# Optimization experiments

Hardware: AMD Instinct MI355X
Metric: run time of the kernel (lower is better)

The kernel has to match this reference:

```python
import jax, jax.numpy as jnp
import numpy as np

N_NODES = 100000
N_EDGES = 1600000


def gcn_conv(x, src, dst, W, b, n_nodes):
    # PyG GCNConv: h = x @ W; symmetric normalization with self-loops; scatter-add; + bias
    deg = jax.ops.segment_sum(jnp.ones_like(src, dtype=x.dtype), dst, num_segments=n_nodes)
    dinv = jax.lax.rsqrt(jnp.where(deg > 0, deg, 1.0))
    norm = dinv[src] * dinv[dst]              # [E+N]
    h = x @ W                                  # [N, out]
    msg = h[src] * norm[:, None]               # gather + scale (irregular access)
    out = jax.ops.segment_sum(msg, dst, num_segments=n_nodes)  # scatter-add aggregate
    return out + b


def setup_inputs() -> dict:
    key = jax.random.key(0)
    k1, k2, k3, k4 = jax.random.split(key, 4)
    x = jax.random.normal(k1, (N_NODES, 128), dtype=jnp.float32)
    edge_index = jax.random.randint(k2, (2, N_EDGES), 0, N_NODES, dtype=jnp.int64)
    W1 = jax.random.normal(k3, (128, 48), dtype=jnp.float32) * (1.0 / np.sqrt(128))
    b1 = jnp.zeros((48,), dtype=jnp.float32)
    W2 = jax.random.normal(k4, (48, 16), dtype=jnp.float32) * (1.0 / np.sqrt(48))
    b2 = jnp.zeros((16,), dtype=jnp.float32)
    return {"x": x, "edge_index": edge_index, "W1": W1, "b1": b1, "W2": W2, "b2": b2}


def reference(x, edge_index, W1, b1, W2, b2):
    n = x.shape[0]
    loops = jnp.arange(n, dtype=edge_index.dtype)
    src = jnp.concatenate([edge_index[0], loops])  # add self-loops
    dst = jnp.concatenate([edge_index[1], loops])
    h = gcn_conv(x, src, dst, W1, b1, n)
    h = jax.nn.relu(h)
    h = gcn_conv(h, src, dst, W2, b2, n)
    h = jax.nn.relu(h)
    return jax.nn.softmax(h, axis=1)
```

## Files before the change

kernel.cpp:

```cpp
#include <hip/hip_runtime.h>
#include <hip/hip_bf16.h>
#include <hip/hip_fp16.h>


#define TILE 4096

typedef _Float16 half8 __attribute__((ext_vector_type(8)));
typedef float floatx4 __attribute__((ext_vector_type(4)));

__global__ __launch_bounds__(256) void k_bhist(const int* __restrict__ dst, int E,
                                               int* __restrict__ Hw, int nbuck) {
    __shared__ int h[512];
    int t = threadIdx.x;
    for (int i = t; i < nbuck; i += 256) h[i] = 0;
    __syncthreads();
    int base = blockIdx.x * TILE;
#pragma unroll
    for (int r = 0; r < TILE / 1024; ++r) {
        int e = base + (r * 256 + t) * 4;
        if (e + 3 < E) {
            int4 d4 = *(const int4*)(dst + e);
            atomicAdd(&h[d4.x >> 8], 1);
            atomicAdd(&h[d4.y >> 8], 1);
            atomicAdd(&h[d4.z >> 8], 1);
            atomicAdd(&h[d4.w >> 8], 1);
        } else {
            for (int k = 0; k < 4; ++k)
                if (e + k < E) atomicAdd(&h[dst[e + k] >> 8], 1);
        }
    }
    __syncthreads();
    for (int i = t; i < nbuck; i += 256) Hw[blockIdx.x * nbuck + i] = h[i];
}

__global__ __launch_bounds__(256) void k_bsum(const int* __restrict__ Hw, int nTiles,
                                              int nbuck, int* __restrict__ btot) {
    int wid = (blockIdx.x * 256 + threadIdx.x) >> 6;
    int lane = threadIdx.x & 63;
    if (wid >= nbuck) return;
    int sum = 0;
    for (int tt = lane; tt < nTiles; tt += 64) sum += Hw[tt * nbuck + wid];
#pragma unroll
    for (int off = 32; off; off >>= 1) sum += __shfl_down(sum, off);
    if (lane == 0) btot[wid] = sum;
}

__global__ __launch_bounds__(256) void k_boff(int* __restrict__ Hw, int nTiles,
                                              int nbuck, const int* __restrict__ btot,
                                              int* __restrict__ bstart) {
    int wid = (blockIdx.x * 256 + threadIdx.x) >> 6;
    int lane = threadIdx.x & 63;
    if (wid >= nbuck) return;
    int ps = 0;
    for (int j = lane; j < wid; j += 64) ps += btot[j];
#pragma unroll
    for (int off = 32; off; off >>= 1) ps += __shfl_down(ps, off);
    int prefix = __shfl(ps, 0);
    if (lane == 0) {
        bstart[wid] = prefix;
        if (wid == nbuck - 1) bstart[nbuck] = prefix + btot[wid];
    }
    int running = prefix;
    for (int chunk = 0; chunk < nTiles; chunk += 64) {
        int tt = chunk + lane;
        int v = (tt < nTiles) ? Hw[tt * nbuck + wid] : 0;
        int incl = v;
#pragma unroll
        for (int off = 1; off < 64; off <<= 1) {
            int u = __shfl_up(incl, off);
            if (lane >= off) incl += u;
        }
        if (tt < nTiles) Hw[tt * nbuck + wid] = running + (incl - v);
        running += __shfl(incl, 63);
    }
}

__global__ __launch_bounds__(256) void k_bscatter(const int* __restrict__ ei, int E,
                                                  const int* __restrict__ Hw, int nbuck,
                                                  int* __restrict__ ebuf) {
    __shared__ int cur[512];
    int t = threadIdx.x;
    for (int i = t; i < nbuck; i += 256) cur[i] = Hw[blockIdx.x * nbuck + i];
    __syncthreads();
    int base = blockIdx.x * TILE;
    bool al = (E & 3) == 0;
#pragma unroll
    for (int r = 0; r < TILE / 1024; ++r) {
        int e = base + (r * 256 + t) * 4;
        if (al && e + 3 < E) {
            int4 s4 = *(const int4*)(ei + e);
            int4 d4 = *(const int4*)(ei + E + e);
            int p0 = atomicAdd(&cur[d4.x >> 8], 1);
            ebuf[p0] = s4.x | ((d4.x & 255) << 17);
            int p1 = atomicAdd(&cur[d4.y >> 8], 1);
            ebuf[p1] = s4.y | ((d4.y & 255) << 17);
            int p2 = atomicAdd(&cur[d4.z >> 8], 1);
            ebuf[p2] = s4.z | ((d4.z & 255) << 17);
            int p3 = atomicAdd(&cur[d4.w >> 8], 1);
            ebuf[p3] = s4.w | ((d4.w & 255) << 17);
        } else {
            for (int k = 0; k < 4; ++k) {
                int ek = e + k;
                if (ek < E) {
                    int s = ei[ek];
                    int d = ei[E + ek];
                    int pos = atomicAdd(&cur[d >> 8], 1);
                    ebuf[pos] = s | ((d & 255) << 17);
                }
            }
        }
    }
}

__global__ __launch_bounds__(256) void k_csrfill(const int* __restrict__ ebuf,
                                                 const int* __restrict__ bstart,
                                                 int* __restrict__ csr,
                                                 int* __restrict__ rowstart,
                                                 float* __restrict__ dinv, int N) {
    __shared__ int lcnt[256];
    __shared__ int lscan[256];
    __shared__ int lcur[256];
    int t = threadIdx.x;
    int nodebase = blockIdx.x << 8;
    int segs = bstart[blockIdx.x];
    int sege = bstart[blockIdx.x + 1];
    int vstart = (segs + 3) & ~3;
    if (vstart > sege) vstart = sege;
    int vend = sege & ~3;
    if (vend < vstart) vend = vstart;
    lcnt[t] = 0;
    __syncthreads();
    for (int i = segs + t; i < vstart; i += 256)
        atomicAdd(&lcnt[((unsigned)ebuf[i]) >> 17], 1);
    for (int i = vstart + t * 4; i < vend; i += 1024) {
        int4 p4 = *(const int4*)(ebuf + i);
        atomicAdd(&lcnt[((unsigned)p4.x) >> 17], 1);
        atomicAdd(&lcnt[((unsigned)p4.y) >> 17], 1);
        atomicAdd(&lcnt[((unsigned)p4.z) >> 17], 1);
        atomicAdd(&lcnt[((unsigned)p4.w) >> 17], 1);
    }
    for (int i = vend + t; i < sege; i += 256)
        atomicAdd(&lcnt[((unsigned)ebuf[i]) >> 17], 1);
    __syncthreads();
    int v = lcnt[t];
    lscan[t] = v;
    __syncthreads();
    for (int off = 1; off < 256; off <<= 1) {
        int tmp = (t >= off) ? lscan[t - off] : 0;
        __syncthreads();
        lscan[t] += tmp;
        __syncthreads();
    }
    int excl = lscan[t] - v;
    int node = nodebase + t;
    int rs = segs + excl;
    if (node < N) {
        rowstart[node] = rs;
        dinv[node] = rsqrtf((float)(v + 1));
        if (node == N - 1) rowstart[N] = rs + v;
    }
    lcur[t] = rs;
    __syncthreads();
    for (int i = segs + t; i < vstart; i += 256) {
        int pk = ebuf[i];
        int pos = atomicAdd(&lcur[((unsigned)pk) >> 17], 1);
        csr[pos] = pk & 0x1FFFF;
    }
    for (int i = vstart + t * 4; i < vend; i += 1024) {
        int4 p4 = *(const int4*)(ebuf + i);
        int pos0 = atomicAdd(&lcur[((unsigned)p4.x) >> 17], 1);
        csr[pos0] = p4.x & 0x1FFFF;
        int pos1 = atomicAdd(&lcur[((unsigned)p4.y) >> 17], 1);
        csr[pos1] = p4.y & 0x1FFFF;
        int pos2 = atomicAdd(&lcur[((unsigned)p4.z) >> 17], 1);
        csr[pos2] = p4.z & 0x1FFFF;
        int pos3 = atomicAdd(&lcur[((unsigned)p4.w) >> 17], 1);
        csr[pos3] = p4.w & 0x1FFFF;
    }
    for (int i = vend + t; i < sege; i += 256) {
        int pk = ebuf[i];
        int pos = atomicAdd(&lcur[((unsigned)pk) >> 17], 1);
        csr[pos] = pk & 0x1FFFF;
    }
}

__global__ __launch_bounds__(256) void k_gemm1(const float* __restrict__ x,
                                               const float* __restrict__ W1,
                                               const float* __restrict__ dinv,
                                               __half* __restrict__ h1p, int N) {
    __shared__ _Float16 wt[48 * 136];
    int t = threadIdx.x;
    for (int i = t; i < 128 * 48; i += 256) {
        int k = i / 48, c = i % 48;
        wt[c * 136 + k] = (_Float16)W1[i];
    }
    __syncthreads();

    int wave = t >> 6, lane = t & 63;
    int g = lane >> 4;
    int rtile = blockIdx.x * 64 + wave * 16;
    int rowA = rtile + (lane & 15);
    const float* xrow = x + (size_t)(rowA < N ? rowA : N - 1) * 128;
    int c0 = lane & 15;

    floatx4 acc[3];
#pragma unroll
    for (int nt = 0; nt < 3; ++nt)
#pragma unroll
        for (int q = 0; q < 4; ++q) acc[nt][q] = 0.f;

#pragma unroll
    for (int kc = 0; kc < 4; ++kc) {
        int k0 = kc * 32 + g * 8;
        float4 a0 = *(const float4*)(xrow + k0);
        float4 a1 = *(const float4*)(xrow + k0 + 4);
        half8 a;
        a[0] = (_Float16)a0.x; a[1] = (_Float16)a0.y;
        a[2] = (_Float16)a0.z; a[3] = (_Float16)a0.w;
        a[4] = (_Float16)a1.x; a[5] = (_Float16)a1.y;
        a[6] = (_Float16)a1.z; a[7] = (_Float16)a1.w;
#pragma unroll
        for (int nt = 0; nt < 3; ++nt) {
            half8 b = *(const half8*)(&wt[(nt * 16 + c0) * 136 + k0]);
            acc[nt] = __builtin_amdgcn_mfma_f32_16x16x32_f16(a, b, acc[nt], 0, 0, 0);
        }
    }

    int rbase = rtile + g * 4;
#pragma unroll
    for (int j = 0; j < 4; ++j) {
        int r = rbase + j;
        if (r < N) {
            float dr = dinv[r];
#pragma unroll
            for (int nt = 0; nt < 3; ++nt)
                h1p[(size_t)r * 48 + nt * 16 + c0] = __float2half(acc[nt][j] * dr);
        }
    }
}

__global__ __launch_bounds__(256) void k_agg1(const __half* __restrict__ h1p,
                                              const int* __restrict__ csr,
                                              const int* __restrict__ rowstart,
                                              const float* __restrict__ dinv,
                                              const float* __restrict__ b1,
                                              __half* __restrict__ r1h, int N) {
    int wave = threadIdx.x >> 6;
    int lane = threadIdx.x & 63;
    int v = blockIdx.x * 4 + wave;
    if (v >= N) return;
    int grp = lane >> 3;
    int sub = lane & 7;

    int start = rowstart[v];
    int d = rowstart[v + 1] - start;
    float dv = dinv[v];
    const int* cs = csr + start;
    const char* h1b = (const char*)h1p;

    float acc[8] = {0.f, 0.f, 0.f, 0.f, 0.f, 0.f, 0.f, 0.f};

    for (int base = 0; base < d; base += 64) {
        int sreg = (base + lane < d) ? cs[base + lane] : 0;
        int nb = min(64, d - base);
        for (int j = 0; j < 8 && j * 8 < nb; ++j) {
            int s = __shfl(sreg, j * 8 + grp);
            if (j * 8 + grp < nb && sub < 6) {
                float4 rv = *(const float4*)(h1b + (size_t)s * 96 + sub * 16);
                const __half2* hp = (const __half2*)&rv;
#pragma unroll
                for (int q = 0; q < 4; ++q) {
                    float2 f = __half22float2(hp[q]);
                    acc[q * 2] += f.x;
                    acc[q * 2 + 1] += f.y;
                }
            }
        }
    }
#pragma unroll
    for (int i = 0; i < 8; ++i) {
        acc[i] += __shfl_xor(acc[i], 8);
        acc[i] += __shfl_xor(acc[i], 16);
        acc[i] += __shfl_xor(acc[i], 32);
    }
    if (grp == 0 && sub < 6) {
        float4 sv = *(const float4*)(h1b + (size_t)v * 96 + sub * 16);
        const __half2* hp = (const __half2*)&sv;
        __half2 ob[4];
#pragma unroll
        for (int q = 0; q < 4; ++q) {
            float2 sf = __half22float2(hp[q]);
            int fi = sub * 8 + q * 2;
            float o0 = fmaxf(dv * (acc[q * 2] + sf.x) + b1[fi], 0.f);
            float o1 = fmaxf(dv * (acc[q * 2 + 1] + sf.y) + b1[fi + 1], 0.f);
            ob[q] = __floats2half2_rn(o0, o1);
        }
        *(float4*)((char*)r1h + (size_t)v * 96 + sub * 16) = *(const float4*)ob;
    }
}

__global__ __launch_bounds__(256) void k_gemm2(const __half* __restrict__ r1h,
                                               const float* __restrict__ W2,
                                               const float* __restrict__ dinv,
                                               __half* __restrict__ h2p, int N) {
    __shared__ float w2s[48 * 16];
    int t = threadIdx.x;
    for (int i = t; i < 768; i += 256) w2s[i] = W2[i];
    __syncthreads();
    int flat = blockIdx.x * 256 + t;
    int row = flat >> 2;
    int cg = (flat & 3) * 4;
    if (row >= N) return;
    float4 acc = make_float4(0.f, 0.f, 0.f, 0.f);
    const __half2* xr = (const __half2*)((const char*)r1h + (size_t)row * 96);
#pragma unroll 4
    for (int kk = 0; kk < 24; ++kk) {
        float2 a = __half22float2(xr[kk]);
        float4 b0 = *(const float4*)(w2s + (2 * kk) * 16 + cg);
        float4 b1v = *(const float4*)(w2s + (2 * kk + 1) * 16 + cg);
        acc.x += a.x * b0.x + a.y * b1v.x;
        acc.y += a.x * b0.y + a.y * b1v.y;
        acc.z += a.x * b0.z + a.y * b1v.z;
        acc.w += a.x * b0.w + a.y * b1v.w;
    }
    float dr = dinv[row];
    __half2 h01 = __floats2half2_rn(acc.x * dr, acc.y * dr);
    __half2 h23 = __floats2half2_rn(acc.z * dr, acc.w * dr);
    __half* dst = h2p + (size_t)row * 16 + cg;
    *(__half2*)(dst) = h01;
    *(__half2*)(dst + 2) = h23;
}

__global__ __launch_bounds__(256) void k_agg2(const __half* __restrict__ h2p,
                                              const int* __restrict__ csr,
                                              const int* __restrict__ rowstart,
                                              const float* __restrict__ dinv,
                                              const float* __restrict__ b2,
                                              float* __restrict__ out, int N) {
    int tid = threadIdx.x;
    int lane = tid & 63;
    int hf = lane >> 5;
    int l32 = lane & 31;
    int grp = l32 >> 1;
    int sub = lane & 1;
    int v = (blockIdx.x * 4 + (tid >> 6)) * 2 + hf;
    if (v >= N) return;

    int start = rowstart[v];
    int d = rowstart[v + 1] - start;
    float dv = dinv[v];
    const int* cs = csr + start;
    const char* h2b = (const char*)h2p;

    float acc[8] = {0.f, 0.f, 0.f, 0.f, 0.f, 0.f, 0.f, 0.f};

    for (int base = 0; base < d; base += 32) {
        int sreg = (base + l32 < d) ? cs[base + l32] : 0;
        int nb = min(32, d - base);
        for (int j = 0; j < 2 && j * 16 < nb; ++j) {
            int e = j * 16 + grp;
            int s = __shfl(sreg, (hf << 5) + e);
            if (e < nb) {
                float4 rv = *(const float4*)(h2b + (size_t)s * 32 + sub * 16);
                const __half2* hp = (const __half2*)&rv;
#pragma unroll
                for (int q = 0; q < 4; ++q) {
                    float2 f = __half22float2(hp[q]);
                    acc[q * 2] += f.x;
                    acc[q * 2 + 1] += f.y;
                }
            }
        }
    }
#pragma unroll
    for (int i = 0; i < 8; ++i) {
        acc[i] += __shfl_xor(acc[i], 2);
        acc[i] += __shfl_xor(acc[i], 4);
        acc[i] += __shfl_xor(acc[i], 8);
        acc[i] += __shfl_xor(acc[i], 16);
    }
    if (grp == 0) {
        float4 sv = *(const float4*)(h2b + (size_t)v * 32 + sub * 16);
        const __half2* hp = (const __half2*)&sv;
        float z[8];
#pragma unroll
        for (int q = 0; q < 4; ++q) {
            float2 f = __half22float2(hp[q]);
            z[q * 2]     = fmaxf(dv * (acc[q * 2] + f.x) + b2[sub * 8 + q * 2], 0.f);
            z[q * 2 + 1] = fmaxf(dv * (acc[q * 2 + 1] + f.y) + b2[sub * 8 + q * 2 + 1], 0.f);
        }
        float m8 = z[0];
#pragma unroll
        for (int i = 1; i < 8; ++i) m8 = fmaxf(m8, z[i]);
        float m = fmaxf(m8, __shfl_xor(m8, 1));
        float p[8];
        float s8 = 0.f;
#pragma unroll
        for (int i = 0; i < 8; ++i) { p[i] = __expf(z[i] - m); s8 += p[i]; }
        float inv = 1.f / (s8 + __shfl_xor(s8, 1));
        float4* dst = (float4*)(out + (size_t)v * 16 + sub * 8);
        dst[0] = make_float4(p[0] * inv, p[1] * inv, p[2] * inv, p[3] * inv);
        dst[1] = make_float4(p[4] * inv, p[5] * inv, p[6] * inv, p[7] * inv);
    }
}

extern "C" void kernel_launch(void* const* d_in, const int* in_sizes, int n_in,
                              void* d_out, int out_size, void* d_ws, size_t ws_size,
                              hipStream_t stream) {
    const float* x  = (const float*)d_in[0];
    const int*   ei = (const int*)d_in[1];
    const float* W1 = (const float*)d_in[2];
    const float* b1 = (const float*)d_in[3];
    const float* W2 = (const float*)d_in[4];
    const float* b2 = (const float*)d_in[5];
    float* out = (float*)d_out;

    int N = in_sizes[0] / 128;
    int E = in_sizes[1] / 2;
    int NBK = (N + 255) >> 8;
    int nTiles = (E + TILE - 1) / TILE;

    char* p = (char*)d_ws;
    auto alloc = [&](size_t bytes) -> char* {
        char* q = p;
        p += (bytes + 255) & ~(size_t)255;
        return q;
    };
    int*    rowstart = (int*)alloc((size_t)(N + 1) * 4);
    float*  dinv     = (float*)alloc((size_t)N * 4);
    int*    btot     = (int*)alloc((size_t)NBK * 4);
    int*    bstart   = (int*)alloc((size_t)(NBK + 1) * 4);
    int*    Hw       = (int*)alloc((size_t)nTiles * NBK * 4);
    int*    csr      = (int*)alloc((size_t)E * 4);
    size_t  ovl_sz   = (size_t)N * 48 * 2 > (size_t)E * 4 ? (size_t)N * 48 * 2
                                                          : (size_t)E * 4;
    char*   ovl      = alloc(ovl_sz);
    int*    ebuf     = (int*)ovl;
    __half* h1p      = (__half*)ovl;
    __half* r1h      = (__half*)alloc((size_t)N * 48 * 2);
    __half* h2p      = h1p;

    int wgBuck = (NBK + 3) / 4;

    hipLaunchKernelGGL(k_bhist, dim3(nTiles), dim3(256), 0, stream, ei + E, E, Hw, NBK);
    hipLaunchKernelGGL(k_bsum, dim3(wgBuck), dim3(256), 0, stream, Hw, nTiles, NBK, btot);
    hipLaunchKernelGGL(k_boff, dim3(wgBuck), dim3(256), 0, stream, Hw, nTiles, NBK,
                       btot, bstart);
    hipLaunchKernelGGL(k_bscatter, dim3(nTiles), dim3(256), 0, stream, ei, E, Hw, NBK, ebuf);
    hipLaunchKernelGGL(k_csrfill, dim3(NBK), dim3(256), 0, stream,
                       ebuf, bstart, csr, rowstart, dinv, N);
    hipLaunchKernelGGL(k_gemm1, dim3((N + 63) / 64), dim3(256), 0, stream,
                       x, W1, dinv, h1p, N);
    hipLaunchKernelGGL(k_agg1, dim3((N + 3) / 4), dim3(256), 0, stream,
                       h1p, csr, rowstart, dinv, b1, r1h, N);
    hipLaunchKernelGGL(k_gemm2, dim3((N * 4 + 255) / 256), dim3(256), 0, stream,
                       r1h, W2, dinv, h2p, N);
    hipLaunchKernelGGL(k_agg2, dim3((N + 7) / 8), dim3(256), 0, stream,
                       h2p, csr, rowstart, dinv, b2, out, N);
}
```

Measured before the change: 137.8 us.

## Fuse CSR build kernels into one cooperative kernel with grid syncs

Merges the five graph-preprocessing kernels (histogram, bucket sum, offsets, scatter, CSR fill) into a single cooperative kernel separated by grid-wide syncs. This removes four kernel launch boundaries and their drain gaps. TILE doubles so the grid (~196 blocks) fits co-resident for cooperative launch, which halves the tile blocks and gives each block more serial work. The bucket loops now run on fewer waves, and grid.sync has its own cost.

After: 240.6 us. 74.6% more time.

```diff
diff --git a/kernel.cpp b/kernel.cpp
--- a/kernel.cpp
+++ b/kernel.cpp
@@ -1,186 +1,191 @@
 #include <hip/hip_runtime.h>
 #include <hip/hip_bf16.h>
 #include <hip/hip_fp16.h>
-
-
-#define TILE 4096
+#include <hip/hip_cooperative_groups.h>
+
+namespace cg = cooperative_groups;
+
+
+#define TILE 8192
 
 typedef _Float16 half8 __attribute__((ext_vector_type(8)));
 typedef float floatx4 __attribute__((ext_vector_type(4)));
 
-__global__ __launch_bounds__(256) void k_bhist(const int* __restrict__ dst, int E,
-                                               int* __restrict__ Hw, int nbuck) {
+__global__ __launch_bounds__(256) void k_build(const int* __restrict__ ei, int E,
+                                               int* __restrict__ Hw, int nbuck,
+                                               int nTiles, int* __restrict__ btot,
+                                               int* __restrict__ bstart,
+                                               int* __restrict__ ebuf,
+                                               int* __restrict__ csr,
+                                               int* __restrict__ rowstart,
+                                               float* __restrict__ dinv, int N) {
+    cg::grid_group grid = cg::this_grid();
     __shared__ int h[512];
-    int t = threadIdx.x;
-    for (int i = t; i < nbuck; i += 256) h[i] = 0;
-    __syncthreads();
-    int base = blockIdx.x * TILE;
-#pragma unroll
-    for (int r = 0; r < TILE / 1024; ++r) {
-        int e = base + (r * 256 + t) * 4;
-        if (e + 3 < E) {
-            int4 d4 = *(const int4*)(dst + e);
-            atomicAdd(&h[d4.x >> 8], 1);
-            atomicAdd(&h[d4.y >> 8], 1);
-            atomicAdd(&h[d4.z >> 8], 1);
-            atomicAdd(&h[d4.w >> 8], 1);
-        } else {
-            for (int k = 0; k < 4; ++k)
-                if (e + k < E) atomicAdd(&h[dst[e + k] >> 8], 1);
-        }
-    }
-    __syncthreads();
-    for (int i = t; i < nbuck; i += 256) Hw[blockIdx.x * nbuck + i] = h[i];
-}
-
-__global__ __launch_bounds__(256) void k_bsum(const int* __restrict__ Hw, int nTiles,
-                                              int nbuck, int* __restrict__ btot) {
-    int wid = (blockIdx.x * 256 + threadIdx.x) >> 6;
-    int lane = threadIdx.x & 63;
-    if (wid >= nbuck) return;
-    int sum = 0;
-    for (int tt = lane; tt < nTiles; tt += 64) sum += Hw[tt * nbuck + wid];
-#pragma unroll
-    for (int off = 32; off; off >>= 1) sum += __shfl_down(sum, off);
-    if (lane == 0) btot[wid] = sum;
-}
-
-__global__ __launch_bounds__(256) void k_boff(int* __restrict__ Hw, int nTiles,
-                                              int nbuck, const int* __restrict__ btot,
-                                              int* __restrict__ bstart) {
-    int wid = (blockIdx.x * 256 + threadIdx.x) >> 6;
-    int lane = threadIdx.x & 63;
-    if (wid >= nbuck) return;
-    int ps = 0;
-    for (int j = lane; j < wid; j += 64) ps += btot[j];
-#pragma unroll
-    for (int off = 32; off; off >>= 1) ps += __shfl_down(ps, off);
-    int prefix = __shfl(ps, 0);
-    if (lane == 0) {
-        bstart[wid] = prefix;
-        if (wid == nbuck - 1) bstart[nbuck] = prefix + btot[wid];
-    }
-    int running = prefix;
-    for (int chunk = 0; chunk < nTiles; chunk += 64) {
-        int tt = chunk + lane;
-        int v = (tt < nTiles) ? Hw[tt * nbuck + wid] : 0;
-        int incl = v;
-#pragma unroll
-        for (int off = 1; off < 64; off <<= 1) {
-            int u = __shfl_up(incl, off);
-            if (lane >= off) incl += u;
-        }
-        if (tt < nTiles) Hw[tt * nbuck + wid] = running + (incl - v);
-        running += __shfl(incl, 63);
-    }
-}
-
-__global__ __launch_bounds__(256) void k_bscatter(const int* __restrict__ ei, int E,
-                                                  const int* __restrict__ Hw, int nbuck,
-                                                  int* __restrict__ ebuf) {
-    __shared__ int cur[512];
-    int t = threadIdx.x;
-    for (int i = t; i < nbuck; i += 256) cur[i] = Hw[blockIdx.x * nbuck + i];
-    __syncthreads();
-    int base = blockIdx.x * TILE;
-    bool al = (E & 3) == 0;
-#pragma unroll
-    for (int r = 0; r < TILE / 1024; ++r) {
-        int e = base + (r * 256 + t) * 4;
-        if (al && e + 3 < E) {
-            int4 s4 = *(const int4*)(ei + e);
-            int4 d4 = *(const int4*)(ei + E + e);
-            int p0 = atomicAdd(&cur[d4.x >> 8], 1);
-            ebuf[p0] = s4.x | ((d4.x & 255) << 17);
-            int p1 = atomicAdd(&cur[d4.y >> 8], 1);
-            ebuf[p1] = s4.y | ((d4.y & 255) << 17);
-            int p2 = atomicAdd(&cur[d4.z >> 8], 1);
-            ebuf[p2] = s4.z | ((d4.z & 255) << 17);
-            int p3 = atomicAdd(&cur[d4.w >> 8], 1);
-            ebuf[p3] = s4.w | ((d4.w & 255) << 17);
-        } else {
-            for (int k = 0; k < 4; ++k) {
-                int ek = e + k;
-                if (ek < E) {
-                    int s = ei[ek];
-                    int d = ei[E + ek];
-                    int pos = atomicAdd(&cur[d >> 8], 1);
-                    ebuf[pos] = s | ((d & 255) << 17);
-                }
-            }
-        }
-    }
-}
-
-__global__ __launch_bounds__(256) void k_csrfill(const int* __restrict__ ebuf,
-                                                 const int* __restrict__ bstart,
-                                                 int* __restrict__ csr,
-                                                 int* __restrict__ rowstart,
-                                                 float* __restrict__ dinv, int N) {
     __shared__ int lcnt[256];
     __shared__ int lscan[256];
     __shared__ int lcur[256];
     int t = threadIdx.x;
-    int nodebase = blockIdx.x << 8;
-    int segs = bstart[blockIdx.x];
-    int sege = bstart[blockIdx.x + 1];
-    int vstart = (segs + 3) & ~3;
-    if (vstart > sege) vstart = sege;
-    int vend = sege & ~3;
-    if (vend < vstart) vend = vstart;
-    lcnt[t] = 0;
-    __syncthreads();
-    for (int i = segs + t; i < vstart; i += 256)
-        atomicAdd(&lcnt[((unsigned)ebuf[i]) >> 17], 1);
-    for (int i = vstart + t * 4; i < vend; i += 1024) {
-        int4 p4 = *(const int4*)(ebuf + i);
-        atomicAdd(&lcnt[((unsigned)p4.x) >> 17], 1);
-        atomicAdd(&lcnt[((unsigned)p4.y) >> 17], 1);
-        atomicAdd(&lcnt[((unsigned)p4.z) >> 17], 1);
-        atomicAdd(&lcnt[((unsigned)p4.w) >> 17], 1);
-    }
-    for (int i = vend + t; i < sege; i += 256)
-        atomicAdd(&lcnt[((unsigned)ebuf[i]) >> 17], 1);
-    __syncthreads();
-    int v = lcnt[t];
-    lscan[t] = v;
-    __syncthreads();
-    for (int off = 1; off < 256; off <<= 1) {
-        int tmp = (t >= off) ? lscan[t - off] : 0;
-        __syncthreads();
-        lscan[t] += tmp;
-        __syncthreads();
-    }
-    int excl = lscan[t] - v;
-    int node = nodebase + t;
-    int rs = segs + excl;
-    if (node < N) {
-        rowstart[node] = rs;
-        dinv[node] = rsqrtf((float)(v + 1));
-        if (node == N - 1) rowstart[N] = rs + v;
-    }
-    lcur[t] = rs;
-    __syncthreads();
-    for (int i = segs + t; i < vstart; i += 256) {
-        int pk = ebuf[i];
-        int pos = atomicAdd(&lcur[((unsigned)pk) >> 17], 1);
-        csr[pos] = pk & 0x1FFFF;
-    }
-    for (int i = vstart + t * 4; i < vend; i += 1024) {
-        int4 p4 = *(const int4*)(ebuf + i);
-        int pos0 = atomicAdd(&lcur[((unsigned)p4.x) >> 17], 1);
-        csr[pos0] = p4.x & 0x1FFFF;
-        int pos1 = atomicAdd(&lcur[((unsigned)p4.y) >> 17], 1);
-        csr[pos1] = p4.y & 0x1FFFF;
-        int pos2 = atomicAdd(&lcur[((unsigned)p4.z) >> 17], 1);
-        csr[pos2] = p4.z & 0x1FFFF;
-        int pos3 = atomicAdd(&lcur[((unsigned)p4.w) >> 17], 1);
-        csr[pos3] = p4.w & 0x1FFFF;
-    }
-    for (int i = vend + t; i < sege; i += 256) {
-        int pk = ebuf[i];
-        int pos = atomicAdd(&lcur[((unsigned)pk) >> 17], 1);
-        csr[pos] = pk & 0x1FFFF;
+    const int* dst = ei + E;
+    bool isTile = (int)blockIdx.x < nTiles;
+
+    if (isTile) {
+        for (int i = t; i < nbuck; i += 256) h[i] = 0;
+        __syncthreads();
+        int base = blockIdx.x * TILE;
+#pragma unroll
+        for (int r = 0; r < TILE / 1024; ++r) {
+            int e = base + (r * 256 + t) * 4;
+            if (e + 3 < E) {
+                int4 d4 = *(const int4*)(dst + e);
+                atomicAdd(&h[d4.x >> 8], 1);
+                atomicAdd(&h[d4.y >> 8], 1);
+                atomicAdd(&h[d4.z >> 8], 1);
+                atomicAdd(&h[d4.w >> 8], 1);
+            } else {
+                for (int k = 0; k < 4; ++k)
+                    if (e + k < E) atomicAdd(&h[dst[e + k] >> 8], 1);
+            }
+        }
+        __syncthreads();
+        for (int i = t; i < nbuck; i += 256) Hw[blockIdx.x * nbuck + i] = h[i];
+    }
+    grid.sync();
+
+    int gw = (blockIdx.x * 256 + t) >> 6;
+    int lane = t & 63;
+    int nw = (gridDim.x * 256) >> 6;
+    for (int wid = gw; wid < nbuck; wid += nw) {
+        int sum = 0;
+        for (int tt = lane; tt < nTiles; tt += 64) sum += Hw[tt * nbuck + wid];
+#pragma unroll
+        for (int off = 32; off; off >>= 1) sum += __shfl_down(sum, off);
+        if (lane == 0) btot[wid] = sum;
+    }
+    grid.sync();
+
+    for (int wid = gw; wid < nbuck; wid += nw) {
+        int ps = 0;
+        for (int j = lane; j < wid; j += 64) ps += btot[j];
+#pragma unroll
+        for (int off = 32; off; off >>= 1) ps += __shfl_down(ps, off);
+        int prefix = __shfl(ps, 0);
+        if (lane == 0) {
+            bstart[wid] = prefix;
+            if (wid == nbuck - 1) bstart[nbuck] = prefix + btot[wid];
+        }
+        int running = prefix;
+        for (int chunk = 0; chunk < nTiles; chunk += 64) {
+            int tt = chunk + lane;
+            int v = (tt < nTiles) ? Hw[tt * nbuck + wid] : 0;
+            int incl = v;
+#pragma unroll
+            for (int off = 1; off < 64; off <<= 1) {
+                int u = __shfl_up(incl, off);
+                if (lane >= off) incl += u;
+            }
+            if (tt < nTiles) Hw[tt * nbuck + wid] = running + (incl - v);
+            running += __shfl(incl, 63);
+        }
+    }
+    grid.sync();
+
+    if (isTile) {
+        for (int i = t; i < nbuck; i += 256) h[i] = Hw[blockIdx.x * nbuck + i];
+        __syncthreads();
+        int base = blockIdx.x * TILE;
+        bool al = (E & 3) == 0;
+#pragma unroll
+        for (int r = 0; r < TILE / 1024; ++r) {
+            int e = base + (r * 256 + t) * 4;
+            if (al && e + 3 < E) {
+                int4 s4 = *(const int4*)(ei + e);
+                int4 d4 = *(const int4*)(ei + E + e);
+                int p0 = atomicAdd(&h[d4.x >> 8], 1);
+                ebuf[p0] = s4.x | ((d4.x & 255) << 17);
+                int p1 = atomicAdd(&h[d4.y >> 8], 1);
+                ebuf[p1] = s4.y | ((d4.y & 255) << 17);
+                int p2 = atomicAdd(&h[d4.z >> 8], 1);
+                ebuf[p2] = s4.z | ((d4.z & 255) << 17);
+                int p3 = atomicAdd(&h[d4.w >> 8], 1);
+                ebuf[p3] = s4.w | ((d4.w & 255) << 17);
+            } else {
+                for (int k = 0; k < 4; ++k) {
+                    int ek = e + k;
+                    if (ek < E) {
+                        int s = ei[ek];
+                        int d = ei[E + ek];
+                        int pos = atomicAdd(&h[d >> 8], 1);
+                        ebuf[pos] = s | ((d & 255) << 17);
+                    }
+                }
+            }
+        }
+    }
+    grid.sync();
+
+    for (int b = blockIdx.x; b < nbuck; b += gridDim.x) {
+        int nodebase = b << 8;
+        int segs = bstart[b];
+        int sege = bstart[b + 1];
+        int vstart = (segs + 3) & ~3;
+        if (vstart > sege) vstart = sege;
+        int vend = sege & ~3;
+        if (vend < vstart) vend = vstart;
+        lcnt[t] = 0;
+        __syncthreads();
+        for (int i = segs + t; i < vstart; i += 256)
+            atomicAdd(&lcnt[((unsigned)ebuf[i]) >> 17], 1);
+        for (int i = vstart + t * 4; i < vend; i += 1024) {
+            int4 p4 = *(const int4*)(ebuf + i);
+            atomicAdd(&lcnt[((unsigned)p4.x) >> 17], 1);
+            atomicAdd(&lcnt[((unsigned)p4.y) >> 17], 1);
+            atomicAdd(&lcnt[((unsigned)p4.z) >> 17], 1);
+            atomicAdd(&lcnt[((unsigned)p4.w) >> 17], 1);
+        }
+        for (int i = vend + t; i < sege; i += 256)
+            atomicAdd(&lcnt[((unsigned)ebuf[i]) >> 17], 1);
+        __syncthreads();
+        int v = lcnt[t];
+        lscan[t] = v;
+        __syncthreads();
+        for (int off = 1; off < 256; off <<= 1) {
+            int tmp = (t >= off) ? lscan[t - off] : 0;
+            __syncthreads();
+            lscan[t] += tmp;
+            __syncthreads();
+        }
+        int excl = lscan[t] - v;
+        int node = nodebase + t;
+        int rs = segs + excl;
+        if (node < N) {
+            rowstart[node] = rs;
+            dinv[node] = rsqrtf((float)(v + 1));
+            if (node == N - 1) rowstart[N] = rs + v;
+        }
+        lcur[t] = rs;
+        __syncthreads();
+        for (int i = segs + t; i < vstart; i += 256) {
+            int pk = ebuf[i];
+            int pos = atomicAdd(&lcur[((unsigned)pk) >> 17], 1);
+            csr[pos] = pk & 0x1FFFF;
+        }
+        for (int i = vstart + t * 4; i < vend; i += 1024) {
+            int4 p4 = *(const int4*)(ebuf + i);
+            int pos0 = atomicAdd(&lcur[((unsigned)p4.x) >> 17], 1);
+            csr[pos0] = p4.x & 0x1FFFF;
+            int pos1 = atomicAdd(&lcur[((unsigned)p4.y) >> 17], 1);
+            csr[pos1] = p4.y & 0x1FFFF;
+            int pos2 = atomicAdd(&lcur[((unsigned)p4.z) >> 17], 1);
+            csr[pos2] = p4.z & 0x1FFFF;
+            int pos3 = atomicAdd(&lcur[((unsigned)p4.w) >> 17], 1);
+            csr[pos3] = p4.w & 0x1FFFF;
+        }
+        for (int i = vend + t; i < sege; i += 256) {
+            int pk = ebuf[i];
+            int pos = atomicAdd(&lcur[((unsigned)pk) >> 17], 1);
+            csr[pos] = pk & 0x1FFFF;
+        }
+        __syncthreads();
     }
 }
 
@@ -407,8 +412,8 @@
 extern "C" void kernel_launch(void* const* d_in, const int* in_sizes, int n_in,
                               void* d_out, int out_size, void* d_ws, size_t ws_size,
                               hipStream_t stream) {
+    const int*   ei_c = (const int*)d_in[1];
     const float* x  = (const float*)d_in[0];
-    const int*   ei = (const int*)d_in[1];
     const float* W1 = (const float*)d_in[2];
     const float* b1 = (const float*)d_in[3];
     const float* W2 = (const float*)d_in[4];
@@ -440,15 +445,13 @@
     __half* r1h      = (__half*)alloc((size_t)N * 48 * 2);
     __half* h2p      = h1p;
 
-    int wgBuck = (NBK + 3) / 4;
-
-    hipLaunchKernelGGL(k_bhist, dim3(nTiles), dim3(256), 0, stream, ei + E, E, Hw, NBK);
-    hipLaunchKernelGGL(k_bsum, dim3(wgBuck), dim3(256), 0, stream, Hw, nTiles, NBK, btot);
-    hipLaunchKernelGGL(k_boff, dim3(wgBuck), dim3(256), 0, stream, Hw, nTiles, NBK,
-                       btot, bstart);
-    hipLaunchKernelGGL(k_bscatter, dim3(nTiles), dim3(256), 0, stream, ei, E, Hw, NBK, ebuf);
-    hipLaunchKernelGGL(k_csrfill, dim3(NBK), dim3(256), 0, stream,
-                       ebuf, bstart, csr, rowstart, dinv, N);
+    const int* ei = ei_c;
+    void* bargs[] = {(void*)&ei, (void*)&E, (void*)&Hw, (void*)&NBK,
+                     (void*)&nTiles, (void*)&btot, (void*)&bstart, (void*)&ebuf,
+                     (void*)&csr, (void*)&rowstart, (void*)&dinv, (void*)&N};
+    hipLaunchCooperativeKernel((void*)k_build, dim3(nTiles), dim3(256),
+                               bargs, 0, stream);
+
     hipLaunchKernelGGL(k_gemm1, dim3((N + 63) / 64), dim3(256), 0, stream,
                        x, W1, dinv, h1p, N);
     hipLaunchKernelGGL(k_agg1, dim3((N + 3) / 4), dim3(256), 0, stream,
```
